# Performance work log

Measured on AMD Instinct MI355X. Metric: run time of the kernel, lower is better.

## Reference

```python
import jax, jax.numpy as jnp
import numpy as np
import math

D = 512
CELLS = 6

def _layer_norm(x, eps=1e-5):
    mu = jnp.mean(x, axis=-1, keepdims=True)
    var = jnp.var(x, axis=-1, keepdims=True)
    return (x - mu) * jax.lax.rsqrt(var + eps)

def setup_inputs() -> dict:
    key = jax.random.key(0)
    k1, k2, k3 = jax.random.split(key, 3)
    B, T = 8, 1024
    x = jax.random.normal(k1, (B * CELLS, T, D), dtype=jnp.float32)
    # causal mask: True = masked (strict upper triangle so diagonal stays valid)
    m = jnp.triu(jnp.ones((T, T), dtype=bool), k=1)
    inhibit = jax.random.normal(k2, (CELLS, CELLS), dtype=jnp.float32) * 0.01
    phases = jnp.linspace(0.0, 2.0 * math.pi, CELLS, dtype=jnp.float32)
    ambition = jnp.ones((CELLS, 1), dtype=jnp.float32) * 0.1
    gate = jax.random.normal(k3, (D, D), dtype=jnp.float32) * 0.02
    return {"x": x, "m": m, "gate": gate, "inhibit": inhibit,
            "phases": phases, "ambition": ambition, "B": B, "T": T}

def reference(x, m, gate, inhibit, phases, ambition, B, T):
    d = gate.shape[0]
    C = inhibit.shape[0]
    nx = _layer_norm(x)
    qkv = nx @ gate                                   # (BC, T, d)
    att = jnp.einsum('btd,bsd->bts', qkv, qkv) * (d ** -0.5)
    att = jnp.where(m, -jnp.inf, att)                 # mask broadcasts over batch
    x = x + jax.nn.softmax(att, axis=-1) @ qkv
    sync = x.reshape(B, C, T, d)
    competed = jnp.einsum('bctd,ck->bktd', sync, inhibit)
    x = x + jnp.tanh(competed).reshape(B * C, T, d)
    p = phases.reshape(1, C, 1, 1)
    a = ambition.reshape(1, C, 1, 1)
    pulse = jnp.sin(x.reshape(B, C, T, d) * a + p)
    return x + pulse.reshape(B * C, T, d) * 0.02
```

## Files before the change

### kernel.cpp

```cpp
#include <hip/hip_runtime.h>
#include <math.h>

typedef __attribute__((ext_vector_type(4))) float f32x4;
typedef __attribute__((ext_vector_type(16))) float f32x16;
typedef __attribute__((ext_vector_type(8))) short s16x8;
typedef __attribute__((ext_vector_type(4))) short s16x4;

#define DD 512
#define TT 1024
#define NB 48

__device__ __forceinline__ short f2bf(float f) {
    union { float f; unsigned u; } v; v.f = f;
    unsigned r = v.u + 0x7fffu + ((v.u >> 16) & 1u);
    return (short)(r >> 16);
}

__device__ __forceinline__ void gll16(const void* g, void* l) {
    __builtin_amdgcn_global_load_lds(
        (const __attribute__((address_space(1))) unsigned int*)g,
        (__attribute__((address_space(3))) unsigned int*)l, 16, 0, 0);
}

__device__ __forceinline__ unsigned pk_bf16(float lo, float hi) {
    unsigned r;
    asm("v_cvt_pk_bf16_f32 %0, %1, %2" : "=v"(r) : "v"(lo), "v"(hi));
    return r;
}

__global__ __launch_bounds__(256) void k_ln_stats(const float* __restrict__ x,
                                                  float* __restrict__ stats) {
    int row = blockIdx.x * 4 + (threadIdx.x >> 6);
    int lane = threadIdx.x & 63;
    const float* p = x + (size_t)row * DD + lane * 8;
    f32x4 a = *(const f32x4*)p;
    f32x4 b = *(const f32x4*)(p + 4);
    float s  = a[0]+a[1]+a[2]+a[3]+b[0]+b[1]+b[2]+b[3];
    float ss = a[0]*a[0]+a[1]*a[1]+a[2]*a[2]+a[3]*a[3]
             + b[0]*b[0]+b[1]*b[1]+b[2]*b[2]+b[3]*b[3];
    #pragma unroll
    for (int off = 32; off >= 1; off >>= 1) {
        s  += __shfl_xor(s, off);
        ss += __shfl_xor(ss, off);
    }
    if (lane == 0) {
        float mu  = s * (1.0f/DD);
        float var = ss * (1.0f/DD) - mu*mu;
        float2 st; st.x = mu; st.y = rsqrtf(var + 1e-5f);
        *(float2*)(stats + (size_t)row*2) = st;
    }
}

__global__ __launch_bounds__(256) void k_gate_t(const float* __restrict__ gate,
                                                short* __restrict__ gateT) {
    __shared__ float tile[64][65];
    int k0 = (blockIdx.x >> 3) * 64;
    int n0 = (blockIdx.x & 7) * 64;
    int tid = threadIdx.x;
    #pragma unroll
    for (int i = 0; i < 16; ++i) {
        int f = i*256 + tid;
        int r = f >> 6, c = f & 63;
        tile[r][c] = gate[(size_t)(k0+r)*DD + n0 + c];
    }
    __syncthreads();
    #pragma unroll
    for (int i = 0; i < 16; ++i) {
        int f = i*256 + tid;
        int r = f >> 6, c = f & 63;
        gateT[(size_t)(n0+r)*DD + k0 + c] = f2bf(tile[c][r]);
    }
}

__global__ __launch_bounds__(256,2) void k_qkv(const float* __restrict__ x,
                                               const float* __restrict__ stats,
                                               const short* __restrict__ gateT,
                                               short* __restrict__ qkv,
                                               short* __restrict__ qkvT) {
    __shared__ __align__(16) short As[128][72];
    __shared__ __align__(16) short Bs[128][72];
    int m0 = (blockIdx.x >> 2) * 128;
    int n0 = (blockIdx.x & 3) * 128;
    int tid = threadIdx.x, lane = tid & 63, w = tid >> 6;
    int wr = w >> 1, wc = w & 1;
    int l15 = lane & 15, lg = lane >> 4;
    f32x4 acc[4][4];
    #pragma unroll
    for (int i=0;i<4;i++)
      #pragma unroll
      for (int j=0;j<4;j++)
        acc[i][j] = (f32x4){0.f,0.f,0.f,0.f};
    for (int kt = 0; kt < 8; ++kt) {
        #pragma unroll
        for (int i = 0; i < 8; ++i) {
            int f4 = i*256 + tid;
            int r  = f4 >> 4;
            int kp = (f4 & 15) * 4;
            f32x4 v = *(const f32x4*)(x + (size_t)(m0+r)*DD + kt*64 + kp);
            float2 st = *(const float2*)(stats + (size_t)(m0+r)*2);
            s16x4 h;
            h[0] = f2bf((v[0]-st.x)*st.y);
            h[1] = f2bf((v[1]-st.x)*st.y);
            h[2] = f2bf((v[2]-st.x)*st.y);
            h[3] = f2bf((v[3]-st.x)*st.y);
            *(s16x4*)(&As[r][kp]) = h;
        }
        #pragma unroll
        for (int i = 0; i < 4; ++i) {
            int f8 = i*256 + tid;
            int r  = f8 >> 3;
            int kp = (f8 & 7) * 8;
            *(s16x8*)(&Bs[r][kp]) = *(const s16x8*)(gateT + (size_t)(n0+r)*DD + kt*64 + kp);
        }
        __syncthreads();
        #pragma unroll
        for (int kk = 0; kk < 2; ++kk) {
            s16x8 af[4], bfr[4];
            #pragma unroll
            for (int mi=0;mi<4;mi++)
                af[mi] = *(const s16x8*)(&As[wr*64 + mi*16 + l15][kk*32 + lg*8]);
            #pragma unroll
            for (int ni=0;ni<4;ni++)
                bfr[ni] = *(const s16x8*)(&Bs[wc*64 + ni*16 + l15][kk*32 + lg*8]);
            #pragma unroll
            for (int mi=0;mi<4;mi++)
              #pragma unroll
              for (int ni=0;ni<4;ni++)
                acc[mi][ni] = __builtin_amdgcn_mfma_f32_16x16x32_bf16(af[mi], bfr[ni], acc[mi][ni], 0,0,0);
        }
        __syncthreads();
    }
    #pragma unroll
    for (int mi=0;mi<4;mi++)
      #pragma unroll
      for (int ni=0;ni<4;ni++) {
        int row0 = m0 + wr*64 + mi*16 + lg*4;
        int col  = n0 + wc*64 + ni*16 + l15;
        s16x4 h4;
        #pragma unroll
        for (int r=0;r<4;r++) h4[r] = f2bf(acc[mi][ni][r]);
        #pragma unroll
        for (int r=0;r<4;r++) qkv[(size_t)(row0+r)*DD + col] = h4[r];
        int b2 = row0 >> 10, t0 = row0 & 1023;
        *(s16x4*)(qkvT + (size_t)b2*DD*TT + (size_t)col*TT + t0) = h4;
      }
}

__global__ __launch_bounds__(512,2) void k_attn(const short* __restrict__ qkv,
                                                const short* __restrict__ qkvT,
                                                const float* __restrict__ xin,
                                                float* __restrict__ out) {
    __shared__ __align__(16) short Kt[2][16384];
    __shared__ __align__(16) short Vt[2][16384];
    __shared__ __align__(16) float Sx[8][1024];
    const float scale = 0.044194173824159216f;
    int bid = blockIdx.x;
    int batch = bid % NB;
    int qg = 7 - (bid / NB);
    int tid = threadIdx.x, lane = tid & 63, w = tid >> 6;
    int s = w & 3, dh = w >> 2;
    int l31 = lane & 31, lh = lane >> 5;
    int qb = qg*128 + s*32;
    int qglob = qb + l31;
    const short* gq  = qkv  + (size_t)batch*TT*DD;
    const short* gvt = qkvT + (size_t)batch*DD*TT;

    s16x8 qf[16];
    {
        const short* qrow = gq + (size_t)qglob*DD + dh*256 + lh*8;
        #pragma unroll
        for (int kc=0;kc<16;kc++) qf[kc] = *(const s16x8*)(qrow + kc*16);
    }
    f32x16 o[8];
    #pragma unroll
    for (int m=0;m<8;m++)
        #pragma unroll
        for (int r=0;r<16;r++) o[m][r] = 0.f;
    float m_run = -1e30f, l_run = 0.f;
    int ntile = 4*(qg+1);

    auto stage = [&](int j, int c) {
        int kv0 = j*32;
        const char* ksrc = (const char*)(gq + (size_t)kv0*DD);
        char* kdst = (char*)&Kt[c][0];
        #pragma unroll
        for (int i=0;i<4;i++){
            int o16 = i*8192 + w*1024;
            int ol  = o16 + (lane<<4);
            int go  = ol ^ (((ol>>10)&7)<<4);
            gll16(ksrc + go, kdst + o16);
        }
        const char* vsrc = (const char*)gvt;
        char* vdst = (char*)&Vt[c][0];
        #pragma unroll
        for (int i=0;i<4;i++){
            int o16 = i*8192 + w*1024;
            int ol  = o16 + (lane<<4);
            int d   = ol >> 6, c2 = ol & 63;
            int c2s = c2 ^ (((d>>1)&3)<<4);
            gll16(vsrc + (size_t)d*2048 + (size_t)kv0*2 + c2s, vdst + o16);
        }
    };

    stage(0, 0);
    __syncthreads();
    for (int kj = 0; kj < ntile; ++kj) {
        int cur = kj & 1;
        int kv0 = kj*32;
        if (kj + 1 < ntile) stage(kj+1, (kj+1)&1);
        const char* kbase = (const char*)&Kt[cur][0];
        const char* vbase = (const char*)&Vt[cur][0];
        f32x16 sT;
        #pragma unroll
        for (int r=0;r<16;r++) sT[r] = 0.f;
        #pragma unroll
        for (int kc=0;kc<16;kc++) {
            int boff = (dh*512 + kc*32 + lh*16) ^ ((l31 & 7) << 4);
            s16x8 kf = *(const s16x8*)(kbase + l31*1024 + boff);
            sT = __builtin_amdgcn_mfma_f32_32x32x16_bf16(kf, qf[kc], sT, 0,0,0);
        }
        {
            float* sw = &Sx[w][0];
            int sl = (lane>>1)&3;
            #pragma unroll
            for (int c=0;c<4;c++){
                f32x4 ch = (f32x4){sT[4*c],sT[4*c+1],sT[4*c+2],sT[4*c+3]};
                *(f32x4*)(sw + lane*16 + ((c ^ sl)<<2)) = ch;
            }
        }
        asm volatile("s_waitcnt lgkmcnt(0)\n\ts_barrier" ::: "memory");
        float p[16]; float mx = -1e30f;
        {
            const float* sr = &Sx[w^4][0];
            int sl = (lane>>1)&3;
            #pragma unroll
            for (int c=0;c<4;c++){
                f32x4 pc = *(const f32x4*)(sr + lane*16 + ((c ^ sl)<<2));
                #pragma unroll
                for (int j=0;j<4;j++){
                    int r = 4*c + j;
                    float v = (sT[r] + pc[j]) * scale;
                    int kvr = kv0 + j + 8*c + 4*lh;
                    if (kvr > qglob) v = -1e30f;
                    p[r] = v;
                    mx = fmaxf(mx, v);
                }
            }
        }
        mx = fmaxf(mx, __shfl_xor(mx, 32));
        if (__any(mx > m_run)) {
            float mn = fmaxf(m_run, mx);
            float alpha = __expf(m_run - mn);
            m_run = mn;
            l_run *= alpha;
            #pragma unroll
            for (int m=0;m<8;m++)
                #pragma unroll
                for (int r=0;r<16;r++) o[m][r] *= alpha;
        }
        float ls = 0.f;
        #pragma unroll
        for (int r=0;r<16;r++){ p[r] = __expf(p[r] - m_run); ls += p[r]; }
        ls += __shfl_xor(ls, 32);
        l_run += ls;
        s16x8 pb[2];
        #pragma unroll
        for (int km=0;km<2;km++){
            int b = 8*km;
            unsigned X0 = pk_bf16(p[b+0], p[b+1]);
            unsigned X1 = pk_bf16(p[b+2], p[b+3]);
            unsigned Y0 = pk_bf16(p[b+4], p[b+5]);
            unsigned Y1 = pk_bf16(p[b+6], p[b+7]);
            asm volatile("v_permlane32_swap_b32 %0, %1" : "+v"(X0), "+v"(Y0));
            asm volatile("v_permlane32_swap_b32 %0, %1" : "+v"(X1), "+v"(Y1));
            union { unsigned u[4]; s16x8 v; } pu;
            pu.u[0] = X0; pu.u[1] = X1; pu.u[2] = Y0; pu.u[3] = Y1;
            pb[km] = pu.v;
        }
        __builtin_amdgcn_s_setprio(1);
        #pragma unroll
        for (int m=0;m<8;m++){
            int row = dh*256 + m*32 + l31;
            #pragma unroll
            for (int km=0;km<2;km++){
                int boff = ((km*32 + lh*16) ^ (((row>>1)&3)<<4));
                s16x8 vf = *(const s16x8*)(vbase + (row<<6) + boff);
                o[m] = __builtin_amdgcn_mfma_f32_32x32x16_bf16(vf, pb[km], o[m], 0,0,0);
            }
        }
        __builtin_amdgcn_s_setprio(0);
        __syncthreads();
    }
    float inv = 1.0f / l_run;
    #pragma unroll
    for (int m=0;m<8;m++)
        #pragma unroll
        for (int r=0;r<16;r++) o[m][r] *= inv;
    float* T = (float*)&Kt[0][0] + w*1152;
    #pragma unroll
    for (int m=0;m<8;m++){
        #pragma unroll
        for (int r=0;r<16;r++){
            int dloc = (r&3) + 8*(r>>2) + 4*lh;
            T[l31*36 + dloc] = o[m][r];
        }
        __builtin_amdgcn_s_waitcnt(0);
        #pragma unroll
        for (int p2=0;p2<4;p2++){
            int qr = p2*8 + (lane>>3);
            f32x4 t = *(const f32x4*)(T + qr*36 + (lane&7)*4);
            size_t gofs = ((size_t)batch*TT + qb + qr)*DD + dh*256 + m*32 + (lane&7)*4;
            f32x4 xi = *(const f32x4*)(xin + gofs);
            *(f32x4*)(out + gofs) = t + xi;
        }
        __builtin_amdgcn_s_waitcnt(0);
    }
}

__device__ __forceinline__ float tanh_fast(float x) {
    float e = __expf(2.0f*x);
    return 1.0f - __fdividef(2.0f, e + 1.0f);
}

__global__ __launch_bounds__(256) void k_post(float* __restrict__ xo,
                                              const float* __restrict__ inhibit,
                                              const float* __restrict__ phases,
                                              const float* __restrict__ ambition) {
    int idx = blockIdx.x*256 + threadIdx.x;
    int b = idx >> 17;
    int rem = idx & 131071;
    size_t base = (size_t)b*6*TT*DD + (size_t)(rem >> 7)*DD + (size_t)(rem & 127)*4;
    f32x4 v[6];
    #pragma unroll
    for (int c=0;c<6;c++) v[c] = *(const f32x4*)(xo + base + (size_t)c*TT*DD);
    float inh[36];
    #pragma unroll
    for (int i=0;i<36;i++) inh[i] = inhibit[i];
    #pragma unroll
    for (int k=0;k<6;k++){
        float c0=0.f, c1=0.f, c2=0.f, c3=0.f;
        #pragma unroll
        for (int c=0;c<6;c++){
            float wv = inh[c*6+k];
            c0 += v[c][0]*wv; c1 += v[c][1]*wv;
            c2 += v[c][2]*wv; c3 += v[c][3]*wv;
        }
        float a = ambition[k], ph = phases[k];
        float x0 = v[k][0] + tanh_fast(c0);
        float x1 = v[k][1] + tanh_fast(c1);
        float x2 = v[k][2] + tanh_fast(c2);
        float x3 = v[k][3] + tanh_fast(c3);
        f32x4 ov;
        ov[0] = x0 + __sinf(x0*a + ph)*0.02f;
        ov[1] = x1 + __sinf(x1*a + ph)*0.02f;
        ov[2] = x2 + __sinf(x2*a + ph)*0.02f;
        ov[3] = x3 + __sinf(x3*a + ph)*0.02f;
        *(f32x4*)(xo + base + (size_t)k*TT*DD) = ov;
    }
}

extern "C" void kernel_launch(void* const* d_in, const int* in_sizes, int n_in,
                              void* d_out, int out_size, void* d_ws, size_t ws_size,
                              hipStream_t stream) {
    (void)in_sizes; (void)n_in; (void)out_size; (void)ws_size;
    const float* x        = (const float*)d_in[0];
    const float* gate     = (const float*)d_in[2];
    const float* inhibit  = (const float*)d_in[3];
    const float* phases   = (const float*)d_in[4];
    const float* ambition = (const float*)d_in[5];
    float* out = (float*)d_out;
    char* ws = (char*)d_ws;
    short* qkv   = (short*)(ws);
    short* qkvT  = (short*)(ws + 50331648);
    float* stats = (float*)(ws + 100663296);
    short* gateT = (short*)(ws + 101056512);

    k_ln_stats <<<dim3(12288), dim3(256), 0, stream>>>(x, stats);
    k_gate_t   <<<dim3(64),    dim3(256), 0, stream>>>(gate, gateT);
    k_qkv      <<<dim3(1536),  dim3(256), 0, stream>>>(x, stats, gateT, qkv, qkvT);
    k_attn     <<<dim3(384),   dim3(512), 0, stream>>>(qkv, qkvT, x, out);
    k_post     <<<dim3(4096),  dim3(256), 0, stream>>>(out, inhibit, phases, ambition);
}
```

Measured before the change: 305.3 us.

## Split attention into 64-query blocks with XCD-aware mapping and single-buffered K/V staging

The attention kernel now uses 256-thread blocks covering 64 queries instead of 512-thread blocks covering 128, doubling the grid to 768 blocks. Batches are assigned to XCDs so each XCD's L2 serves a fixed set of six batches. Double-buffered K/V staging is replaced by single buffers, with K reloaded after the S exchange barrier and V reloaded after the PV barrier. Wave-tiles that lie fully above the causal diagonal skip their compute. The QK reduction is also split into two independent accumulators to shorten the MFMA dependency chain. The aim is finer causal load balance, better L2 locality and lower LDS use. The cost is less overlap between loads and compute, because each tile now waits on vmcnt(0) before proceeding.

Result: slower. 390.2 us (+27.8%).

```diff
diff --git a/kernel.cpp b/kernel.cpp
--- a/kernel.cpp
+++ b/kernel.cpp
@@ -146,21 +146,22 @@
       }
 }
 
-__global__ __launch_bounds__(512,2) void k_attn(const short* __restrict__ qkv,
+__global__ __launch_bounds__(256,2) void k_attn(const short* __restrict__ qkv,
                                                 const short* __restrict__ qkvT,
                                                 const float* __restrict__ xin,
                                                 float* __restrict__ out) {
-    __shared__ __align__(16) short Kt[2][16384];
-    __shared__ __align__(16) short Vt[2][16384];
-    __shared__ __align__(16) float Sx[8][1024];
+    __shared__ __align__(16) short Kt[16384];
+    __shared__ __align__(16) short Vt[16384];
+    __shared__ __align__(16) float Sx[4][1024];
     const float scale = 0.044194173824159216f;
     int bid = blockIdx.x;
-    int batch = bid % NB;
-    int qg = 7 - (bid / NB);
+    int xcd = bid & 7, k = bid >> 3;
+    int batch = 6*xcd + (k % 6);
+    int qj = 15 - (k / 6);
     int tid = threadIdx.x, lane = tid & 63, w = tid >> 6;
-    int s = w & 3, dh = w >> 2;
+    int s = w >> 1, dh = w & 1;
     int l31 = lane & 31, lh = lane >> 5;
-    int qb = qg*128 + s*32;
+    int qb = qj*64 + s*32;
     int qglob = qb + l31;
     const short* gq  = qkv  + (size_t)batch*TT*DD;
     const short* gvt = qkvT + (size_t)batch*DD*TT;
@@ -177,24 +178,26 @@
         #pragma unroll
         for (int r=0;r<16;r++) o[m][r] = 0.f;
     float m_run = -1e30f, l_run = 0.f;
-    int ntile = 4*(qg+1);
-
-    auto stage = [&](int j, int c) {
-        int kv0 = j*32;
-        const char* ksrc = (const char*)(gq + (size_t)kv0*DD);
-        char* kdst = (char*)&Kt[c][0];
-        #pragma unroll
-        for (int i=0;i<4;i++){
-            int o16 = i*8192 + w*1024;
+    int ntile = 2*(qj+1);
+
+    auto stageK = [&](int t) {
+        const char* ksrc = (const char*)(gq + (size_t)(t*32)*DD);
+        char* kdst = (char*)&Kt[0];
+        #pragma unroll
+        for (int i=0;i<8;i++){
+            int o16 = i*4096 + w*1024;
             int ol  = o16 + (lane<<4);
             int go  = ol ^ (((ol>>10)&7)<<4);
             gll16(ksrc + go, kdst + o16);
         }
+    };
+    auto stageV = [&](int t) {
+        int kv0 = t*32;
         const char* vsrc = (const char*)gvt;
-        char* vdst = (char*)&Vt[c][0];
-        #pragma unroll
-        for (int i=0;i<4;i++){
-            int o16 = i*8192 + w*1024;
+        char* vdst = (char*)&Vt[0];
+        #pragma unroll
+        for (int i=0;i<8;i++){
+            int o16 = i*4096 + w*1024;
             int ol  = o16 + (lane<<4);
             int d   = ol >> 6, c2 = ol & 63;
             int c2s = c2 ^ (((d>>1)&3)<<4);
@@ -202,101 +205,110 @@
         }
     };
 
-    stage(0, 0);
+    stageK(0); stageV(0);
     __syncthreads();
-    for (int kj = 0; kj < ntile; ++kj) {
-        int cur = kj & 1;
-        int kv0 = kj*32;
-        if (kj + 1 < ntile) stage(kj+1, (kj+1)&1);
-        const char* kbase = (const char*)&Kt[cur][0];
-        const char* vbase = (const char*)&Vt[cur][0];
-        f32x16 sT;
-        #pragma unroll
-        for (int r=0;r<16;r++) sT[r] = 0.f;
-        #pragma unroll
-        for (int kc=0;kc<16;kc++) {
-            int boff = (dh*512 + kc*32 + lh*16) ^ ((l31 & 7) << 4);
-            s16x8 kf = *(const s16x8*)(kbase + l31*1024 + boff);
-            sT = __builtin_amdgcn_mfma_f32_32x32x16_bf16(kf, qf[kc], sT, 0,0,0);
-        }
-        {
+    for (int t = 0; t < ntile; ++t) {
+        int kv0 = t*32;
+        bool act = (kv0 <= qb + 31);
+        const char* kbase = (const char*)&Kt[0];
+        const char* vbase = (const char*)&Vt[0];
+        f32x16 sA, sB;
+        if (act) {
+            #pragma unroll
+            for (int r=0;r<16;r++){ sA[r]=0.f; sB[r]=0.f; }
+            #pragma unroll
+            for (int kc=0;kc<8;kc++) {
+                int b0 = (dh*512 + (2*kc)*32 + lh*16) ^ ((l31 & 7) << 4);
+                int b1 = (dh*512 + (2*kc+1)*32 + lh*16) ^ ((l31 & 7) << 4);
+                s16x8 kf0 = *(const s16x8*)(kbase + l31*1024 + b0);
+                s16x8 kf1 = *(const s16x8*)(kbase + l31*1024 + b1);
+                sA = __builtin_amdgcn_mfma_f32_32x32x16_bf16(kf0, qf[2*kc],   sA, 0,0,0);
+                sB = __builtin_amdgcn_mfma_f32_32x32x16_bf16(kf1, qf[2*kc+1], sB, 0,0,0);
+            }
             float* sw = &Sx[w][0];
             int sl = (lane>>1)&3;
             #pragma unroll
             for (int c=0;c<4;c++){
-                f32x4 ch = (f32x4){sT[4*c],sT[4*c+1],sT[4*c+2],sT[4*c+3]};
+                f32x4 ch = (f32x4){sA[4*c]+sB[4*c], sA[4*c+1]+sB[4*c+1],
+                                   sA[4*c+2]+sB[4*c+2], sA[4*c+3]+sB[4*c+3]};
                 *(f32x4*)(sw + lane*16 + ((c ^ sl)<<2)) = ch;
             }
         }
-        asm volatile("s_waitcnt lgkmcnt(0)\n\ts_barrier" ::: "memory");
-        float p[16]; float mx = -1e30f;
-        {
-            const float* sr = &Sx[w^4][0];
-            int sl = (lane>>1)&3;
-            #pragma unroll
-            for (int c=0;c<4;c++){
-                f32x4 pc = *(const f32x4*)(sr + lane*16 + ((c ^ sl)<<2));
+        asm volatile("s_waitcnt vmcnt(0) lgkmcnt(0)\n\ts_barrier" ::: "memory");
+        if (t + 1 < ntile) stageK(t+1);
+        if (act) {
+            float p[16]; float mx = -1e30f;
+            {
+                const float* sr = &Sx[w^1][0];
+                int sl = (lane>>1)&3;
                 #pragma unroll
-                for (int j=0;j<4;j++){
-                    int r = 4*c + j;
-                    float v = (sT[r] + pc[j]) * scale;
-                    int kvr = kv0 + j + 8*c + 4*lh;
-                    if (kvr > qglob) v = -1e30f;
-                    p[r] = v;
-                    mx = fmaxf(mx, v);
+                for (int c=0;c<4;c++){
+                    f32x4 pc = *(const f32x4*)(sr + lane*16 + ((c ^ sl)<<2));
+                    #pragma unroll
+                    for (int jj=0;jj<4;jj++){
+                        int r = 4*c + jj;
+                        float v;
+                        if (dh == 0) v = (sA[r]+sB[r] + pc[jj]) * scale;
+                        else         v = (sA[r]+sB[r] + pc[jj]) * scale;
+                        int kvr = kv0 + jj + 8*c + 4*lh;
+                        if (kvr > qglob) v = -1e30f;
+                        p[r] = v;
+                        mx = fmaxf(mx, v);
+                    }
                 }
             }
-        }
-        mx = fmaxf(mx, __shfl_xor(mx, 32));
-        if (__any(mx > m_run)) {
-            float mn = fmaxf(m_run, mx);
-            float alpha = __expf(m_run - mn);
-            m_run = mn;
-            l_run *= alpha;
-            #pragma unroll
-            for (int m=0;m<8;m++)
+            mx = fmaxf(mx, __shfl_xor(mx, 32));
+            if (__any(mx > m_run)) {
+                float mn = fmaxf(m_run, mx);
+                float alpha = __expf(m_run - mn);
+                m_run = mn;
+                l_run *= alpha;
                 #pragma unroll
-                for (int r=0;r<16;r++) o[m][r] *= alpha;
-        }
-        float ls = 0.f;
-        #pragma unroll
-        for (int r=0;r<16;r++){ p[r] = __expf(p[r] - m_run); ls += p[r]; }
-        ls += __shfl_xor(ls, 32);
-        l_run += ls;
-        s16x8 pb[2];
-        #pragma unroll
-        for (int km=0;km<2;km++){
-            int b = 8*km;
-            unsigned X0 = pk_bf16(p[b+0], p[b+1]);
-            unsigned X1 = pk_bf16(p[b+2], p[b+3]);
-            unsigned Y0 = pk_bf16(p[b+4], p[b+5]);
-            unsigned Y1 = pk_bf16(p[b+6], p[b+7]);
-            asm volatile("v_permlane32_swap_b32 %0, %1" : "+v"(X0), "+v"(Y0));
-            asm volatile("v_permlane32_swap_b32 %0, %1" : "+v"(X1), "+v"(Y1));
-            union { unsigned u[4]; s16x8 v; } pu;
-            pu.u[0] = X0; pu.u[1] = X1; pu.u[2] = Y0; pu.u[3] = Y1;
-            pb[km] = pu.v;
-        }
-        __builtin_amdgcn_s_setprio(1);
-        #pragma unroll
-        for (int m=0;m<8;m++){
-            int row = dh*256 + m*32 + l31;
+                for (int m=0;m<8;m++)
+                    #pragma unroll
+                    for (int r=0;r<16;r++) o[m][r] *= alpha;
+            }
+            float ls = 0.f;
+            #pragma unroll
+            for (int r=0;r<16;r++){ p[r] = __expf(p[r] - m_run); ls += p[r]; }
+            ls += __shfl_xor(ls, 32);
+            l_run += ls;
+            s16x8 pb[2];
             #pragma unroll
             for (int km=0;km<2;km++){
-                int boff = ((km*32 + lh*16) ^ (((row>>1)&3)<<4));
-                s16x8 vf = *(const s16x8*)(vbase + (row<<6) + boff);
-                o[m] = __builtin_amdgcn_mfma_f32_32x32x16_bf16(vf, pb[km], o[m], 0,0,0);
-            }
-        }
-        __builtin_amdgcn_s_setprio(0);
+                int b = 8*km;
+                unsigned X0 = pk_bf16(p[b+0], p[b+1]);
+                unsigned X1 = pk_bf16(p[b+2], p[b+3]);
+                unsigned Y0 = pk_bf16(p[b+4], p[b+5]);
+                unsigned Y1 = pk_bf16(p[b+6], p[b+7]);
+                asm volatile("v_permlane32_swap_b32 %0, %1" : "+v"(X0), "+v"(Y0));
+                asm volatile("v_permlane32_swap_b32 %0, %1" : "+v"(X1), "+v"(Y1));
+                union { unsigned u[4]; s16x8 v; } pu;
+                pu.u[0] = X0; pu.u[1] = X1; pu.u[2] = Y0; pu.u[3] = Y1;
+                pb[km] = pu.v;
+            }
+            __builtin_amdgcn_s_setprio(1);
+            #pragma unroll
+            for (int m=0;m<8;m++){
+                int row = dh*256 + m*32 + l31;
+                #pragma unroll
+                for (int km=0;km<2;km++){
+                    int boff = ((km*32 + lh*16) ^ (((row>>1)&3)<<4));
+                    s16x8 vf = *(const s16x8*)(vbase + (row<<6) + boff);
+                    o[m] = __builtin_amdgcn_mfma_f32_32x32x16_bf16(vf, pb[km], o[m], 0,0,0);
+                }
+            }
+            __builtin_amdgcn_s_setprio(0);
+        }
         __syncthreads();
+        if (t + 1 < ntile) stageV(t+1);
     }
     float inv = 1.0f / l_run;
     #pragma unroll
     for (int m=0;m<8;m++)
         #pragma unroll
         for (int r=0;r<16;r++) o[m][r] *= inv;
-    float* T = (float*)&Kt[0][0] + w*1152;
+    float* T = (float*)&Kt[0] + w*1152;
     #pragma unroll
     for (int m=0;m<8;m++){
         #pragma unroll
@@ -308,10 +320,10 @@
         #pragma unroll
         for (int p2=0;p2<4;p2++){
             int qr = p2*8 + (lane>>3);
-            f32x4 t = *(const f32x4*)(T + qr*36 + (lane&7)*4);
+            f32x4 tv = *(const f32x4*)(T + qr*36 + (lane&7)*4);
             size_t gofs = ((size_t)batch*TT + qb + qr)*DD + dh*256 + m*32 + (lane&7)*4;
             f32x4 xi = *(const f32x4*)(xin + gofs);
-            *(f32x4*)(out + gofs) = t + xi;
+            *(f32x4*)(out + gofs) = tv + xi;
         }
         __builtin_amdgcn_s_waitcnt(0);
     }
@@ -378,6 +390,6 @@
     k_ln_stats <<<dim3(12288), dim3(256), 0, stream>>>(x, stats);
     k_gate_t   <<<dim3(64),    dim3(256), 0, stream>>>(gate, gateT);
     k_qkv      <<<dim3(1536),  dim3(256), 0, stream>>>(x, stats, gateT, qkv, qkvT);
-    k_attn     <<<dim3(384),   dim3(512), 0, stream>>>(qkv, qkvT, x, out);
+    k_attn     <<<dim3(768),   dim3(256), 0, stream>>>(qkv, qkvT, x, out);
     k_post     <<<dim3(4096),  dim3(256), 0, stream>>>(out, inhibit, phases, ambition);
 }
```
